# Kernel tuning notes

Hardware: AMD Instinct MI355X
Metric: run time of the kernel (lower is better)

The kernel has to match this reference:

```python
import jax, jax.numpy as jnp
import numpy as np

B = 128      # trees per batch
D = 10       # tree depth (perfect binary tree)
L = 2 ** D   # leaves per tree
V = 50000    # vocab
E = 300      # embed size
C = 5        # num classes


def setup_inputs() -> dict:
    key = jax.random.key(0)
    k0, k1, k2, k3 = jax.random.split(key, 4)
    return {
        "word_ids": jax.random.randint(k0, (B, L), 0, V),
        "embedding": jax.random.normal(k1, (V, E), jnp.float32) * 0.02,
        "W_w": jax.random.normal(k2, (E, 2 * E), jnp.float32) * (1.0 / np.sqrt(2 * E)),
        "W_b": jnp.zeros((E,), jnp.float32),
        "P_w": jax.random.normal(k3, (C, E), jnp.float32) * (1.0 / np.sqrt(E)),
        "P_b": jnp.zeros((C,), jnp.float32),
    }


def reference(word_ids, embedding, W_w, W_b, P_w, P_b):
    # Leaf nodes: relu(Embedding(word))  -> [B, L, E]
    h = jax.nn.relu(embedding[word_ids])
    # projection of every node (torch Linear: x @ W.T + b)
    logits = [jnp.einsum("bne,ce->bnc", h, P_w) + P_b]
    # Combine same-depth sibling pairs level by level (D fixed levels).
    for _ in range(D):
        pair = jnp.concatenate([h[:, 0::2], h[:, 1::2]], axis=-1)  # [B, n/2, 2E]
        h = jax.nn.relu(jnp.einsum("bnf,ef->bne", pair, W_w) + W_b)  # [B, n/2, E]
        logits.append(jnp.einsum("bne,ce->bnc", h, P_w) + P_b)
    # All node logits, leaves first then each internal level up to the root.
    return jnp.concatenate(logits, axis=1)  # [B, 2L-1, C]
```

## Files before the change

### kernel.cpp

```cpp
#include <hip/hip_runtime.h>
#include <hip/hip_bf16.h>

#define B_ 128
#define E_ 300
#define C_ 5
#define NODES 2047

typedef __attribute__((ext_vector_type(8))) short short8;
typedef __attribute__((ext_vector_type(4))) float f32x4;
typedef __hip_bfloat16 bf16;

__device__ __forceinline__ short f2bs(float v) {
  bf16 b = (bf16)v;
  return *reinterpret_cast<short*>(&b);
}

__device__ __forceinline__ short8 pack_relu(f32x4 v0, f32x4 v1) {
  short8 s;
#pragma unroll
  for (int j = 0; j < 4; j++) s[j] = f2bs(fmaxf(v0[j], 0.f));
#pragma unroll
  for (int j = 0; j < 4; j++) s[4 + j] = f2bs(fmaxf(v1[j], 0.f));
  return s;
}

#define HSROW(base, r) ((base) + (r) * 312)

#define PROJ_A(rowptr, ks, k0)                               \
  ((ks) == 9 && half >= 2 ? (short8){0, 0, 0, 0, 0, 0, 0, 0} \
                          : *(const short8*)((rowptr) + (k0)))

__global__ __launch_bounds__(256) void prep_k(
    const float* __restrict__ emb, const float* __restrict__ Ww,
    const float* __restrict__ Pw, bf16* __restrict__ T, bf16* __restrict__ Wf,
    bf16* __restrict__ Pqf, bf16* __restrict__ Ppf, int V) {
  int idx = blockIdx.x * 256 + threadIdx.x;
  int tchunks = V * 38;
  if (idx < tchunks) {
    int v = idx / 38, c = idx % 38;
    const float* src = emb + (size_t)v * E_ + c * 8;
    f32x4 v0 = *(const f32x4*)src;
    f32x4 v1 = (c == 37) ? (f32x4){0.f, 0.f, 0.f, 0.f}
                         : *(const f32x4*)(src + 4);
    *(short8*)(T + (size_t)v * 304 + c * 8) = pack_relu(v0, v1);
  }
  if (idx < 20 * 19 * 64) {
    int wnt = idx / 1216, rem = idx % 1216;
    int ks = rem >> 6, l = rem & 63;
    int n = wnt * 16 + (l & 15);
    int k0 = ks * 32 + (l >> 4) * 8;
    short8 v;
#pragma unroll
    for (int j = 0; j < 8; j++) {
      int k = k0 + j;
      float x = 0.f;
      if (n < E_) {
        if (k < E_) x = Ww[n * 600 + k];
        else if (k >= 304 && k < 604) x = Ww[n * 600 + k - 4];
      }
      v[j] = f2bs(x);
    }
    *(short8*)(Wf + (size_t)idx * 8) = v;
  }
  if (idx < 2 * 19 * 64) {
    int p = idx / 1216, rem = idx % 1216;
    int ks = rem >> 6, l = rem & 63;
    int q = l & 15;
    int k0 = ks * 32 + (l >> 4) * 8;
    short8 v;
#pragma unroll
    for (int j = 0; j < 8; j++) {
      int e = k0 + j - 304 * p;
      float x = (q < C_ && e >= 0 && e < E_) ? Pw[q * E_ + e] : 0.f;
      v[j] = f2bs(x);
    }
    *(short8*)(Pqf + (size_t)idx * 8) = v;
  }
  if (idx < 10 * 64) {
    int ks = idx >> 6, l = idx & 63;
    int q = l & 15;
    int k0 = ks * 32 + (l >> 4) * 8;
    short8 v;
#pragma unroll
    for (int j = 0; j < 8; j++) {
      int e = k0 + j;
      float x = (q < C_ && e < E_) ? Pw[q * E_ + e] : 0.f;
      v[j] = f2bs(x);
    }
    *(short8*)(Ppf + (size_t)idx * 8) = v;
  }
}

__global__ __launch_bounds__(512, 2) void fused_l1_k(
    const int* __restrict__ wid, const bf16* __restrict__ T,
    const bf16* __restrict__ Wf, const float* __restrict__ Wb,
    const bf16* __restrict__ Pqf, const bf16* __restrict__ Ppf,
    const float* __restrict__ Pb, bf16* __restrict__ h1f,
    float* __restrict__ out) {
  __shared__ short ldsA[64 * 616 + 64];
  int tid = threadIdx.x;
  int m0 = blockIdx.x * 64;

  for (int i = tid; i < 64 * 76; i += 512) {
    int r = i / 76, c2 = i % 76;
    int par = c2 >= 38 ? 1 : 0;
    int c = c2 - 38 * par;
    int word = wid[2 * (m0 + r) + par];
    short8 v = *(const short8*)(T + (size_t)word * 304 + c * 8);
    *(short8*)&ldsA[r * 616 + par * 304 + c * 8] = v;
  }
  __syncthreads();

  int w = tid >> 6, l = tid & 63, q = l & 15, half = l >> 4;
  int wg = w & 3, wh = w >> 2;
  int ab0 = ((wh * 2 + 0) * 16 + q) * 616;
  int ab1 = ((wh * 2 + 1) * 16 + q) * 616;
  int abL = ((w & 3) * 16 + q) * 616;
  int pL = w >> 2;

  f32x4 acc[2][5];
#pragma unroll
  for (int rt = 0; rt < 2; rt++)
#pragma unroll
    for (int nt = 0; nt < 5; nt++) acc[rt][nt] = (f32x4){0.f, 0.f, 0.f, 0.f};
  f32x4 pacc = (f32x4){0.f, 0.f, 0.f, 0.f};

#pragma unroll 2
  for (int ks = 0; ks < 19; ks++) {
    int k0 = ks * 32 + half * 8;
    short8 a0 = *(const short8*)&ldsA[ab0 + k0];
    short8 a1 = *(const short8*)&ldsA[ab1 + k0];
    short8 al = *(const short8*)&ldsA[abL + k0];
    short8 pq = *(const short8*)(Pqf + ((size_t)(pL * 19 + ks) * 64 + l) * 8);
    pacc = __builtin_amdgcn_mfma_f32_16x16x32_bf16(al, pq, pacc, 0, 0, 0);
#pragma unroll
    for (int nt = 0; nt < 5; nt++) {
      short8 b = *(const short8*)(Wf +
          ((size_t)((5 * wg + nt) * 19 + ks) * 64 + l) * 8);
      acc[0][nt] =
          __builtin_amdgcn_mfma_f32_16x16x32_bf16(a0, b, acc[0][nt], 0, 0, 0);
      acc[1][nt] =
          __builtin_amdgcn_mfma_f32_16x16x32_bf16(a1, b, acc[1][nt], 0, 0, 0);
    }
  }
  __syncthreads();

#pragma unroll
  for (int nt = 0; nt < 5; nt++) {
    int n = wg * 80 + nt * 16 + q;
    float wb = (n < E_) ? Wb[n] : 0.f;
    if (n < 304) {
#pragma unroll
      for (int rt = 0; rt < 2; rt++)
#pragma unroll
        for (int j = 0; j < 4; j++) {
          int rl = (wh * 2 + rt) * 16 + half * 4 + j;
          HSROW(ldsA, rl)[n] = f2bs(fmaxf(acc[rt][nt][j] + wb, 0.f));
        }
    }
  }
  if (q < C_) {
    float pb = Pb[q];
#pragma unroll
    for (int j = 0; j < 4; j++) {
      int row = m0 + (w & 3) * 16 + half * 4 + j;
      int leaf = 2 * row + pL;
      out[((size_t)(leaf >> 10) * NODES + (leaf & 1023)) * C_ + q] =
          pacc[j] + pb;
    }
  }
  __syncthreads();

  for (int i = tid; i < 2 * 19 * 64; i += 512) {
    int gl = i / 1216, rem = i % 1216;
    int ks = rem >> 6, ll = rem & 63;
    int qq = ll & 15, hh = ll >> 4;
    int k0 = ks * 32 + hh * 8;
    int sel = k0 >= 304 ? 1 : 0;
    int e = k0 - 304 * sel;
    int lr = 2 * (gl * 16 + qq) + sel;
    short8 v = *(const short8*)&HSROW(ldsA, lr)[e];
    *(short8*)(h1f + (((size_t)((m0 >> 5) + gl) * 19 + ks) * 64 + ll) * 8) = v;
  }
  if (w < 4) {
    f32x4 pc = (f32x4){0.f, 0.f, 0.f, 0.f};
#pragma unroll
    for (int ks = 0; ks < 10; ks++) {
      int k0 = ks * 32 + half * 8;
      short8 a = PROJ_A(HSROW(ldsA, 16 * w + q), ks, k0);
      short8 b = *(const short8*)(Ppf + ((size_t)ks * 64 + l) * 8);
      pc = __builtin_amdgcn_mfma_f32_16x16x32_bf16(a, b, pc, 0, 0, 0);
    }
    if (q < C_) {
      float pb = Pb[q];
#pragma unroll
      for (int j = 0; j < 4; j++) {
        int m = m0 + w * 16 + half * 4 + j;
        out[((size_t)(m >> 9) * NODES + 1024 + (m & 511)) * C_ + q] =
            pc[j] + pb;
      }
    }
  }
}

template <int RT>
__global__ __launch_bounds__(512, 2) void combine_k(
    const bf16* __restrict__ hin_f, const bf16* __restrict__ Wf,
    const float* __restrict__ Wb, const bf16* __restrict__ Ppf,
    const float* __restrict__ Pb, bf16* __restrict__ hout_f,
    float* __restrict__ out, int node_off, int nshift) {
  const int HR = RT / 2;
  __shared__ short hsO[RT * 16 * 312 + 64];
  int tid = threadIdx.x;
  int w = tid >> 6, l = tid & 63, q = l & 15, half = l >> 4;
  int wg = w & 3, wh = w >> 2;
  int m0 = blockIdx.x * (RT * 16);
  int g0 = (m0 >> 4) + wh * HR;

  f32x4 acc[HR][5];
#pragma unroll
  for (int rt = 0; rt < HR; rt++)
#pragma unroll
    for (int nt = 0; nt < 5; nt++) acc[rt][nt] = (f32x4){0.f, 0.f, 0.f, 0.f};

#pragma unroll 2
  for (int ks = 0; ks < 19; ks++) {
    short8 a[HR];
#pragma unroll
    for (int rt = 0; rt < HR; rt++)
      a[rt] = *(const short8*)(hin_f +
          (((size_t)(g0 + rt) * 19 + ks) * 64 + l) * 8);
#pragma unroll
    for (int nt = 0; nt < 5; nt++) {
      short8 b = *(const short8*)(Wf +
          ((size_t)((5 * wg + nt) * 19 + ks) * 64 + l) * 8);
#pragma unroll
      for (int rt = 0; rt < HR; rt++)
        acc[rt][nt] = __builtin_amdgcn_mfma_f32_16x16x32_bf16(
            a[rt], b, acc[rt][nt], 0, 0, 0);
    }
  }

#pragma unroll
  for (int nt = 0; nt < 5; nt++) {
    int n = wg * 80 + nt * 16 + q;
    float wb = (n < E_) ? Wb[n] : 0.f;
    if (n < 304) {
#pragma unroll
      for (int rt = 0; rt < HR; rt++)
#pragma unroll
        for (int j = 0; j < 4; j++) {
          int rl = (wh * HR + rt) * 16 + half * 4 + j;
          HSROW(hsO, rl)[n] = f2bs(fmaxf(acc[rt][nt][j] + wb, 0.f));
        }
    }
  }
  __syncthreads();

  for (int i = tid; i < (RT / 2) * 1216; i += 512) {
    int gl = i / 1216, rem = i % 1216;
    int ks = rem >> 6, ll = rem & 63;
    int qq = ll & 15, hh = ll >> 4;
    int k0 = ks * 32 + hh * 8;
    int sel = k0 >= 304 ? 1 : 0;
    int e = k0 - 304 * sel;
    int lr = 2 * (gl * 16 + qq) + sel;
    short8 v = *(const short8*)&HSROW(hsO, lr)[e];
    *(short8*)(hout_f +
               (((size_t)((m0 >> 5) + gl) * 19 + ks) * 64 + ll) * 8) = v;
  }
  if (w < RT) {
    f32x4 pacc = (f32x4){0.f, 0.f, 0.f, 0.f};
#pragma unroll
    for (int ks = 0; ks < 10; ks++) {
      int k0 = ks * 32 + half * 8;
      short8 a = PROJ_A(HSROW(hsO, 16 * w + q), ks, k0);
      short8 b = *(const short8*)(Ppf + ((size_t)ks * 64 + l) * 8);
      pacc = __builtin_amdgcn_mfma_f32_16x16x32_bf16(a, b, pacc, 0, 0, 0);
    }
    if (q < C_) {
      float pb = Pb[q];
#pragma unroll
      for (int j = 0; j < 4; j++) {
        size_t m = m0 + w * 16 + half * 4 + j;
        size_t b_ = m >> nshift;
        size_t n = m & (((size_t)1 << nshift) - 1);
        out[((size_t)b_ * NODES + node_off + n) * C_ + q] = pacc[j] + pb;
      }
    }
  }
}

extern "C" void kernel_launch(void* const* d_in, const int* in_sizes, int n_in,
                              void* d_out, int out_size, void* d_ws,
                              size_t ws_size, hipStream_t stream) {
  const int* wid = (const int*)d_in[0];
  const float* emb = (const float*)d_in[1];
  const float* Ww = (const float*)d_in[2];
  const float* Wb = (const float*)d_in[3];
  const float* Pw = (const float*)d_in[4];
  const float* Pb = (const float*)d_in[5];
  float* out = (float*)d_out;
  int V = in_sizes[1] / E_;

  bf16* hA = (bf16*)d_ws;
  bf16* hB = hA + (size_t)B_ * 512 * 304;
  bf16* Wf = hB + (size_t)B_ * 256 * 304;
  bf16* Pqf = Wf + (size_t)20 * 19 * 512;
  bf16* Ppf = Pqf + (size_t)2 * 19 * 512;
  bf16* T = Ppf + (size_t)10 * 512;

  int tchunks = V * 38;
  prep_k<<<(tchunks + 255) / 256, 256, 0, stream>>>(emb, Ww, Pw, T, Wf, Pqf,
                                                    Ppf, V);
  fused_l1_k<<<1024, 512, 0, stream>>>(wid, T, Wf, Wb, Pqf, Ppf, Pb, hA, out);
  combine_k<4><<<512, 512, 0, stream>>>(hA, Wf, Wb, Ppf, Pb, hB, out, 1536, 8);
  combine_k<4><<<256, 512, 0, stream>>>(hB, Wf, Wb, Ppf, Pb, hA, out, 1792, 7);
  combine_k<2><<<256, 512, 0, stream>>>(hA, Wf, Wb, Ppf, Pb, hB, out, 1920, 6);
  combine_k<2><<<128, 512, 0, stream>>>(hB, Wf, Wb, Ppf, Pb, hA, out, 1984, 5);
  combine_k<2><<<64, 512, 0, stream>>>(hA, Wf, Wb, Ppf, Pb, hB, out, 2016, 4);
  combine_k<2><<<32, 512, 0, stream>>>(hB, Wf, Wb, Ppf, Pb, hA, out, 2032, 3);
  combine_k<2><<<16, 512, 0, stream>>>(hA, Wf, Wb, Ppf, Pb, hB, out, 2040, 2);
  combine_k<2><<<8, 512, 0, stream>>>(hB, Wf, Wb, Ppf, Pb, hA, out, 2044, 1);
  combine_k<2><<<4, 512, 0, stream>>>(hA, Wf, Wb, Ppf, Pb, hB, out, 2046, 0);
}
```

Baseline: 202.7 us.

## Double row tile per block in level-1 and early combine kernels

The fused leaf/level-1 kernel now processes 128 rows per block instead of 64, and each wave computes four row tiles against each loaded W fragment, so global weight loads are reused across more MFMAs. The early combine levels switch to an 8-row-tile variant with half the blocks. Launch bounds drop the two-blocks-per-CU hint to allow more registers, with the LDS footprint doubling. The cost is lower occupancy and fewer blocks, which may leave CUs idle on the small later levels.

New measurement: 250.3 us. +23.5%, slower.

```diff
diff --git a/kernel.cpp b/kernel.cpp
--- a/kernel.cpp
+++ b/kernel.cpp
@@ -91,17 +91,19 @@
   }
 }
 
-__global__ __launch_bounds__(512, 2) void fused_l1_k(
+__global__ __launch_bounds__(512) void fused_l1_k(
     const int* __restrict__ wid, const bf16* __restrict__ T,
     const bf16* __restrict__ Wf, const float* __restrict__ Wb,
     const bf16* __restrict__ Pqf, const bf16* __restrict__ Ppf,
     const float* __restrict__ Pb, bf16* __restrict__ h1f,
     float* __restrict__ out) {
-  __shared__ short ldsA[64 * 616 + 64];
+  __shared__ short ldsA[128 * 616 + 64];
   int tid = threadIdx.x;
-  int m0 = blockIdx.x * 64;
-
-  for (int i = tid; i < 64 * 76; i += 512) {
+  int m0 = blockIdx.x * 128;
+
+#pragma unroll 2
+  for (int it = 0; it < 19; ++it) {
+    int i = it * 512 + tid;
     int r = i / 76, c2 = i % 76;
     int par = c2 >= 38 ? 1 : 0;
     int c = c2 - 38 * par;
@@ -113,26 +115,31 @@
 
   int w = tid >> 6, l = tid & 63, q = l & 15, half = l >> 4;
   int wg = w & 3, wh = w >> 2;
-  int ab0 = ((wh * 2 + 0) * 16 + q) * 616;
-  int ab1 = ((wh * 2 + 1) * 16 + q) * 616;
-  int abL = ((w & 3) * 16 + q) * 616;
-  int pL = w >> 2;
-
-  f32x4 acc[2][5];
-#pragma unroll
-  for (int rt = 0; rt < 2; rt++)
+  int ab[4];
+#pragma unroll
+  for (int rt = 0; rt < 4; rt++) ab[rt] = ((wh * 4 + rt) * 16 + q) * 616;
+  int abL = (w * 16 + q) * 616;
+
+  f32x4 acc[4][5];
+#pragma unroll
+  for (int rt = 0; rt < 4; rt++)
 #pragma unroll
     for (int nt = 0; nt < 5; nt++) acc[rt][nt] = (f32x4){0.f, 0.f, 0.f, 0.f};
-  f32x4 pacc = (f32x4){0.f, 0.f, 0.f, 0.f};
+  f32x4 pacc0 = (f32x4){0.f, 0.f, 0.f, 0.f};
+  f32x4 pacc1 = (f32x4){0.f, 0.f, 0.f, 0.f};
 
 #pragma unroll 2
   for (int ks = 0; ks < 19; ks++) {
     int k0 = ks * 32 + half * 8;
-    short8 a0 = *(const short8*)&ldsA[ab0 + k0];
-    short8 a1 = *(const short8*)&ldsA[ab1 + k0];
+    short8 a0 = *(const short8*)&ldsA[ab[0] + k0];
+    short8 a1 = *(const short8*)&ldsA[ab[1] + k0];
+    short8 a2 = *(const short8*)&ldsA[ab[2] + k0];
+    short8 a3 = *(const short8*)&ldsA[ab[3] + k0];
     short8 al = *(const short8*)&ldsA[abL + k0];
-    short8 pq = *(const short8*)(Pqf + ((size_t)(pL * 19 + ks) * 64 + l) * 8);
-    pacc = __builtin_amdgcn_mfma_f32_16x16x32_bf16(al, pq, pacc, 0, 0, 0);
+    short8 pq0 = *(const short8*)(Pqf + ((size_t)(0 * 19 + ks) * 64 + l) * 8);
+    short8 pq1 = *(const short8*)(Pqf + ((size_t)(1 * 19 + ks) * 64 + l) * 8);
+    pacc0 = __builtin_amdgcn_mfma_f32_16x16x32_bf16(al, pq0, pacc0, 0, 0, 0);
+    pacc1 = __builtin_amdgcn_mfma_f32_16x16x32_bf16(al, pq1, pacc1, 0, 0, 0);
 #pragma unroll
     for (int nt = 0; nt < 5; nt++) {
       short8 b = *(const short8*)(Wf +
@@ -141,6 +148,10 @@
           __builtin_amdgcn_mfma_f32_16x16x32_bf16(a0, b, acc[0][nt], 0, 0, 0);
       acc[1][nt] =
           __builtin_amdgcn_mfma_f32_16x16x32_bf16(a1, b, acc[1][nt], 0, 0, 0);
+      acc[2][nt] =
+          __builtin_amdgcn_mfma_f32_16x16x32_bf16(a2, b, acc[2][nt], 0, 0, 0);
+      acc[3][nt] =
+          __builtin_amdgcn_mfma_f32_16x16x32_bf16(a3, b, acc[3][nt], 0, 0, 0);
     }
   }
   __syncthreads();
@@ -151,10 +162,10 @@
     float wb = (n < E_) ? Wb[n] : 0.f;
     if (n < 304) {
 #pragma unroll
-      for (int rt = 0; rt < 2; rt++)
+      for (int rt = 0; rt < 4; rt++)
 #pragma unroll
         for (int j = 0; j < 4; j++) {
-          int rl = (wh * 2 + rt) * 16 + half * 4 + j;
+          int rl = (wh * 4 + rt) * 16 + half * 4 + j;
           HSROW(ldsA, rl)[n] = f2bs(fmaxf(acc[rt][nt][j] + wb, 0.f));
         }
     }
@@ -163,15 +174,17 @@
     float pb = Pb[q];
 #pragma unroll
     for (int j = 0; j < 4; j++) {
-      int row = m0 + (w & 3) * 16 + half * 4 + j;
-      int leaf = 2 * row + pL;
-      out[((size_t)(leaf >> 10) * NODES + (leaf & 1023)) * C_ + q] =
-          pacc[j] + pb;
+      int row = m0 + w * 16 + half * 4 + j;
+      int leaf0 = 2 * row, leaf1 = 2 * row + 1;
+      out[((size_t)(leaf0 >> 10) * NODES + (leaf0 & 1023)) * C_ + q] =
+          pacc0[j] + pb;
+      out[((size_t)(leaf1 >> 10) * NODES + (leaf1 & 1023)) * C_ + q] =
+          pacc1[j] + pb;
     }
   }
   __syncthreads();
 
-  for (int i = tid; i < 2 * 19 * 64; i += 512) {
+  for (int i = tid; i < 4 * 1216; i += 512) {
     int gl = i / 1216, rem = i % 1216;
     int ks = rem >> 6, ll = rem & 63;
     int qq = ll & 15, hh = ll >> 4;
@@ -182,7 +195,7 @@
     short8 v = *(const short8*)&HSROW(ldsA, lr)[e];
     *(short8*)(h1f + (((size_t)((m0 >> 5) + gl) * 19 + ks) * 64 + ll) * 8) = v;
   }
-  if (w < 4) {
+  {
     f32x4 pc = (f32x4){0.f, 0.f, 0.f, 0.f};
 #pragma unroll
     for (int ks = 0; ks < 10; ks++) {
@@ -204,7 +217,7 @@
 }
 
 template <int RT>
-__global__ __launch_bounds__(512, 2) void combine_k(
+__global__ __launch_bounds__(512) void combine_k(
     const bf16* __restrict__ hin_f, const bf16* __restrict__ Wf,
     const float* __restrict__ Wb, const bf16* __restrict__ Ppf,
     const float* __restrict__ Pb, bf16* __restrict__ hout_f,
@@ -313,11 +326,11 @@
   int tchunks = V * 38;
   prep_k<<<(tchunks + 255) / 256, 256, 0, stream>>>(emb, Ww, Pw, T, Wf, Pqf,
                                                     Ppf, V);
-  fused_l1_k<<<1024, 512, 0, stream>>>(wid, T, Wf, Wb, Pqf, Ppf, Pb, hA, out);
-  combine_k<4><<<512, 512, 0, stream>>>(hA, Wf, Wb, Ppf, Pb, hB, out, 1536, 8);
-  combine_k<4><<<256, 512, 0, stream>>>(hB, Wf, Wb, Ppf, Pb, hA, out, 1792, 7);
-  combine_k<2><<<256, 512, 0, stream>>>(hA, Wf, Wb, Ppf, Pb, hB, out, 1920, 6);
-  combine_k<2><<<128, 512, 0, stream>>>(hB, Wf, Wb, Ppf, Pb, hA, out, 1984, 5);
+  fused_l1_k<<<512, 512, 0, stream>>>(wid, T, Wf, Wb, Pqf, Ppf, Pb, hA, out);
+  combine_k<8><<<256, 512, 0, stream>>>(hA, Wf, Wb, Ppf, Pb, hB, out, 1536, 8);
+  combine_k<8><<<128, 512, 0, stream>>>(hB, Wf, Wb, Ppf, Pb, hA, out, 1792, 7);
+  combine_k<8><<<64, 512, 0, stream>>>(hA, Wf, Wb, Ppf, Pb, hB, out, 1920, 6);
+  combine_k<8><<<32, 512, 0, stream>>>(hB, Wf, Wb, Ppf, Pb, hA, out, 1984, 5);
   combine_k<2><<<64, 512, 0, stream>>>(hA, Wf, Wb, Ppf, Pb, hB, out, 2016, 4);
   combine_k<2><<<32, 512, 0, stream>>>(hB, Wf, Wb, Ppf, Pb, hA, out, 2032, 3);
   combine_k<2><<<16, 512, 0, stream>>>(hA, Wf, Wb, Ppf, Pb, hB, out, 2040, 2);
```

## Fuse pairs of upper tree levels into one kernel using LDS intermediates

Applied to the files above, without the earlier changes.

Replaces the six small per-level combine launches for the top levels with three launches of a new dual-level kernel. Each block computes one level from global fragments, keeps the result in LDS, then computes the next level and both projections from it before writing the next fragment layout. This is meant to remove launch overhead and a global round trip of intermediates at levels with little parallelism. In exchange, each block does a longer sequential chain of work, and the grids are very small, down to 8 blocks, so most of the GPU sits idle.

New measurement: 295.5 us. 45.7% more time.

```diff
diff --git a/kernel.cpp b/kernel.cpp
--- a/kernel.cpp
+++ b/kernel.cpp
@@ -291,6 +291,144 @@
   }
 }
 
+__global__ __launch_bounds__(256, 4) void dual_k(
+    const bf16* __restrict__ hin_f, const bf16* __restrict__ Wf,
+    const float* __restrict__ Wb, const bf16* __restrict__ Ppf,
+    const float* __restrict__ Pb, bf16* __restrict__ hout_f,
+    float* __restrict__ out, int off1, int ns1, int off2, int ns2, int last) {
+  __shared__ short lds[48 * 312 + 16];
+  short* t1 = lds;
+  short* t2 = lds + 32 * 312;
+  int tid = threadIdx.x;
+  int w = tid >> 6, l = tid & 63, q = l & 15, half = l >> 4;
+  int b = blockIdx.x;
+  int g0 = 2 * b;
+
+  f32x4 acc[2][5];
+#pragma unroll
+  for (int rt = 0; rt < 2; rt++)
+#pragma unroll
+    for (int nt = 0; nt < 5; nt++) acc[rt][nt] = (f32x4){0.f, 0.f, 0.f, 0.f};
+
+#pragma unroll 2
+  for (int ks = 0; ks < 19; ks++) {
+    short8 a0 = *(const short8*)(hin_f +
+        (((size_t)g0 * 19 + ks) * 64 + l) * 8);
+    short8 a1 = *(const short8*)(hin_f +
+        (((size_t)(g0 + 1) * 19 + ks) * 64 + l) * 8);
+#pragma unroll
+    for (int nt = 0; nt < 5; nt++) {
+      short8 bfr = *(const short8*)(Wf +
+          ((size_t)((5 * w + nt) * 19 + ks) * 64 + l) * 8);
+      acc[0][nt] =
+          __builtin_amdgcn_mfma_f32_16x16x32_bf16(a0, bfr, acc[0][nt], 0, 0, 0);
+      acc[1][nt] =
+          __builtin_amdgcn_mfma_f32_16x16x32_bf16(a1, bfr, acc[1][nt], 0, 0, 0);
+    }
+  }
+
+#pragma unroll
+  for (int nt = 0; nt < 5; nt++) {
+    int n = w * 80 + nt * 16 + q;
+    float wb = (n < E_) ? Wb[n] : 0.f;
+    if (n < 304) {
+#pragma unroll
+      for (int rt = 0; rt < 2; rt++)
+#pragma unroll
+        for (int j = 0; j < 4; j++) {
+          int rl = rt * 16 + half * 4 + j;
+          HSROW(t1, rl)[n] = f2bs(fmaxf(acc[rt][nt][j] + wb, 0.f));
+        }
+    }
+  }
+  __syncthreads();
+
+  if (w < 2) {
+    f32x4 pacc = (f32x4){0.f, 0.f, 0.f, 0.f};
+#pragma unroll
+    for (int ks = 0; ks < 10; ks++) {
+      int k0 = ks * 32 + half * 8;
+      short8 a = PROJ_A(HSROW(t1, 16 * w + q), ks, k0);
+      short8 bfr = *(const short8*)(Ppf + ((size_t)ks * 64 + l) * 8);
+      pacc = __builtin_amdgcn_mfma_f32_16x16x32_bf16(a, bfr, pacc, 0, 0, 0);
+    }
+    if (q < C_) {
+      float pb = Pb[q];
+#pragma unroll
+      for (int j = 0; j < 4; j++) {
+        size_t m = (size_t)b * 32 + w * 16 + half * 4 + j;
+        out[((m >> ns1) * NODES + off1 + (m & (((size_t)1 << ns1) - 1))) * C_ +
+            q] = pacc[j] + pb;
+      }
+    }
+  }
+
+  f32x4 acc2[5];
+#pragma unroll
+  for (int nt = 0; nt < 5; nt++) acc2[nt] = (f32x4){0.f, 0.f, 0.f, 0.f};
+#pragma unroll 2
+  for (int ks = 0; ks < 19; ks++) {
+    int k0 = ks * 32 + half * 8;
+    int sel = k0 >= 304 ? 1 : 0;
+    int e0 = k0 - 304 * sel;
+    short8 a = *(const short8*)&HSROW(t1, 2 * q + sel)[e0];
+#pragma unroll
+    for (int nt = 0; nt < 5; nt++) {
+      short8 bfr = *(const short8*)(Wf +
+          ((size_t)((5 * w + nt) * 19 + ks) * 64 + l) * 8);
+      acc2[nt] =
+          __builtin_amdgcn_mfma_f32_16x16x32_bf16(a, bfr, acc2[nt], 0, 0, 0);
+    }
+  }
+#pragma unroll
+  for (int nt = 0; nt < 5; nt++) {
+    int n = w * 80 + nt * 16 + q;
+    float wb = (n < E_) ? Wb[n] : 0.f;
+    if (n < 304) {
+#pragma unroll
+      for (int j = 0; j < 4; j++) {
+        HSROW(t2, half * 4 + j)[n] = f2bs(fmaxf(acc2[nt][j] + wb, 0.f));
+      }
+    }
+  }
+  __syncthreads();
+
+  if (w == 0) {
+    f32x4 pacc = (f32x4){0.f, 0.f, 0.f, 0.f};
+#pragma unroll
+    for (int ks = 0; ks < 10; ks++) {
+      int k0 = ks * 32 + half * 8;
+      short8 a = PROJ_A(HSROW(t2, q), ks, k0);
+      short8 bfr = *(const short8*)(Ppf + ((size_t)ks * 64 + l) * 8);
+      pacc = __builtin_amdgcn_mfma_f32_16x16x32_bf16(a, bfr, pacc, 0, 0, 0);
+    }
+    if (q < C_) {
+      float pb = Pb[q];
+#pragma unroll
+      for (int j = 0; j < 4; j++) {
+        size_t m = (size_t)b * 16 + half * 4 + j;
+        out[((m >> ns2) * NODES + off2 + (m & (((size_t)1 << ns2) - 1))) * C_ +
+            q] = pacc[j] + pb;
+      }
+    }
+  }
+  if (!last) {
+    int g = b >> 1, hi = b & 1;
+    for (int i = tid; i < 1216; i += 256) {
+      int ks = i >> 6, ll = i & 63;
+      int qq = ll & 15, hh = ll >> 4;
+      if ((qq >> 3) == hi) {
+        int k0 = ks * 32 + hh * 8;
+        int sel = k0 >= 304 ? 1 : 0;
+        int e = k0 - 304 * sel;
+        int lr2 = 2 * (qq & 7) + sel;
+        short8 v = *(const short8*)&HSROW(t2, lr2)[e];
+        *(short8*)(hout_f + (((size_t)g * 19 + ks) * 64 + ll) * 8) = v;
+      }
+    }
+  }
+}
+
 extern "C" void kernel_launch(void* const* d_in, const int* in_sizes, int n_in,
                               void* d_out, int out_size, void* d_ws,
                               size_t ws_size, hipStream_t stream) {
@@ -317,10 +455,10 @@
   combine_k<4><<<512, 512, 0, stream>>>(hA, Wf, Wb, Ppf, Pb, hB, out, 1536, 8);
   combine_k<4><<<256, 512, 0, stream>>>(hB, Wf, Wb, Ppf, Pb, hA, out, 1792, 7);
   combine_k<2><<<256, 512, 0, stream>>>(hA, Wf, Wb, Ppf, Pb, hB, out, 1920, 6);
-  combine_k<2><<<128, 512, 0, stream>>>(hB, Wf, Wb, Ppf, Pb, hA, out, 1984, 5);
-  combine_k<2><<<64, 512, 0, stream>>>(hA, Wf, Wb, Ppf, Pb, hB, out, 2016, 4);
-  combine_k<2><<<32, 512, 0, stream>>>(hB, Wf, Wb, Ppf, Pb, hA, out, 2032, 3);
-  combine_k<2><<<16, 512, 0, stream>>>(hA, Wf, Wb, Ppf, Pb, hB, out, 2040, 2);
-  combine_k<2><<<8, 512, 0, stream>>>(hB, Wf, Wb, Ppf, Pb, hA, out, 2044, 1);
-  combine_k<2><<<4, 512, 0, stream>>>(hA, Wf, Wb, Ppf, Pb, hB, out, 2046, 0);
-}
+  dual_k<<<128, 256, 0, stream>>>(hB, Wf, Wb, Ppf, Pb, hA, out,
+                                  1984, 5, 2016, 4, 0);
+  dual_k<<<32, 256, 0, stream>>>(hA, Wf, Wb, Ppf, Pb, hB, out,
+                                 2032, 3, 2040, 2, 0);
+  dual_k<<<8, 256, 0, stream>>>(hB, Wf, Wb, Ppf, Pb, hA, out,
+                                2044, 1, 2046, 0, 1);
+}
```
